# Optimization experiments

Measured on AMD Instinct MI355X. Metric: run time of the kernel, lower is better.

The kernel has to match this reference:

```python
import jax, jax.numpy as jnp
import numpy as np


def _hungarian(cost):
    """Kuhn-Munkres / Jonker-Volgenant shortest augmenting path on a square
    cost matrix (numpy, float). Returns col index assigned to each row,
    identical to scipy.optimize.linear_sum_assignment's col_ind."""
    n = cost.shape[0]
    INF = np.inf
    u = np.zeros(n + 1)
    v = np.zeros(n + 1)
    p = np.zeros(n + 1, dtype=np.int64)    # p[j] = row matched to col j (1-based)
    way = np.zeros(n + 1, dtype=np.int64)
    for i in range(1, n + 1):
        p[0] = i
        j0 = 0
        minv = np.full(n + 1, INF)
        used = np.zeros(n + 1, dtype=bool)
        while True:
            used[j0] = True
            i0 = p[j0]
            cur = cost[i0 - 1] - u[i0] - v[1:]
            m1 = minv[1:]
            w1 = way[1:]
            upd = (~used[1:]) & (cur < m1)
            m1[upd] = cur[upd]
            w1[upd] = j0
            masked = np.where(used[1:], INF, m1)
            j1 = int(np.argmin(masked)) + 1
            delta = masked[j1 - 1]
            uidx = np.nonzero(used)[0]
            u[p[uidx]] += delta
            v[uidx] -= delta
            minv[~used] -= delta
            j0 = j1
            if p[j0] == 0:
                break
        # augment along the alternating path
        while True:
            j1 = way[j0]
            p[j0] = p[j1]
            j0 = j1
            if j0 == 0:
                break
    ans = np.zeros(n, dtype=np.int64)
    for j in range(1, n + 1):
        ans[p[j] - 1] = j - 1
    return ans


def _cdist(a, b):
    # [B,K,D] x [B,K,D] -> [B,K,K] pairwise L2 distances (torch.cdist p=2)
    aa = jnp.sum(a * a, axis=-1)[:, :, None]
    bb = jnp.sum(b * b, axis=-1)[:, None, :]
    ab = jnp.einsum('bkd,bjd->bkj', a, b)
    return jnp.sqrt(jnp.clip(aa + bb - 2.0 * ab, 0.0))


def setup_inputs() -> dict:
    key = jax.random.key(0)
    k1, k2, k3 = jax.random.split(key, 3)
    B, K, D, N = 64, 32, 256, 16384
    return {
        'slots_t': jax.random.normal(k1, (B, K, D), jnp.float32),
        'slots_t1': jax.random.normal(k2, (B, K, D), jnp.float32),
        'masks_t': jax.random.uniform(k3, (B, N, K), jnp.float32),
    }


def reference(slots_t, slots_t1, masks_t):
    # cost matrix (l2) and per-batch optimal assignment (host-side, like torch)
    cost = np.asarray(_cdist(slots_t, slots_t1))          # [B,K,K]
    match = jnp.asarray(
        np.stack([_hungarian(cost[b]) for b in range(cost.shape[0])]))  # [B,K]
    # gather matched slots from t+1
    matched = jnp.take_along_axis(slots_t1, match[:, :, None], axis=1)  # [B,K,D]
    loss = jnp.sum((slots_t - matched) ** 2, axis=-1)                   # [B,K]
    # slot-utilization weighting from masks
    util = masks_t.sum(axis=1)                                          # [B,K]
    util = util / util.sum(axis=1, keepdims=True)
    loss = loss * util
    return loss.mean()
```

## Files before the change

kernel.cpp:

```cpp
#include <hip/hip_runtime.h>
#include <math.h>

#define BATCH 64
#define KSL   32
#define DIM   256
#define NMASK 16384

template<int CTRL>
__device__ __forceinline__ double dpp_mov_f64(double x) {
  union { double d; int i[2]; } a, r;
  a.d = x;
  r.i[0] = __builtin_amdgcn_update_dpp(a.i[0], a.i[0], CTRL, 0xF, 0xF, false);
  r.i[1] = __builtin_amdgcn_update_dpp(a.i[1], a.i[1], CTRL, 0xF, 0xF, false);
  return r.d;
}

__device__ __forceinline__ double readlane_f64(double x, int lane) {
  union { double d; unsigned long long u; } a; a.d = x;
  int lo = __builtin_amdgcn_readlane((int)(a.u & 0xFFFFFFFFull), lane);
  int hi = __builtin_amdgcn_readlane((int)(a.u >> 32), lane);
  union { unsigned long long u; double d; } r;
  r.u = ((unsigned long long)(unsigned)hi << 32) | (unsigned)lo;
  return r.d;
}

__global__ __launch_bounds__(256) void fused_kernel(
    const float* __restrict__ slots_t, const float* __restrict__ slots_t1,
    const float* __restrict__ masks,
    int* __restrict__ match, float* __restrict__ partial) {
  int tid = threadIdx.x;
  if (blockIdx.x < BATCH) {
    int b = blockIdx.x;
    __shared__ float as[KSL][64];
    __shared__ float bs[KSL][65];
    __shared__ float cs[KSL][KSL];
    const float* ab = slots_t  + (size_t)b * KSL * DIM;
    const float* bb = slots_t1 + (size_t)b * KSL * DIM;

    float acc[4] = {0.f, 0.f, 0.f, 0.f};
    for (int c = 0; c < DIM / 64; ++c) {
      __syncthreads();
      for (int e = tid; e < KSL * 64; e += 256) {
        int kk = e >> 6, dd = e & 63;
        as[kk][dd] = ab[kk * DIM + c * 64 + dd];
        bs[kk][dd] = bb[kk * DIM + c * 64 + dd];
      }
      __syncthreads();
      #pragma unroll
      for (int p4 = 0; p4 < 4; ++p4) {
        int id = p4 * 256 + tid;
        int i = id >> 5, j = id & 31;
        float s = acc[p4];
        #pragma unroll
        for (int dd = 0; dd < 64; ++dd) {
          float df = as[i][dd] - bs[j][dd];
          s = fmaf(df, df, s);
        }
        acc[p4] = s;
      }
    }
    __syncthreads();
    #pragma unroll
    for (int p4 = 0; p4 < 4; ++p4) {
      int id = p4 * 256 + tid;
      cs[id >> 5][id & 31] = sqrtf(acc[p4]);
    }
    __syncthreads();
    if (tid >= 32) return;

    const int col = tid;
    double v = 0.0, up = 0.0;
    int pcol = 0;
    unsigned freemask = 0xFFFFFFFFu;
    for (int i = 1; i <= KSL; ++i) {
      double u_i = 0.0;
      int used = 0;
      int i0 = i;
      double u0 = 0.0;
      for (;;) {
        double cur = (double)cs[i0 - 1][col] - u0 - v;
        double masked = used ? __builtin_inf() : cur;
        double m = masked;
        m = fmin(m, dpp_mov_f64<0xB1>(m));
        m = fmin(m, dpp_mov_f64<0x4E>(m));
        m = fmin(m, dpp_mov_f64<0x141>(m));
        m = fmin(m, dpp_mov_f64<0x140>(m));
        m = fmin(m, dpp_mov_f64<0x142>(m));
        double delta = readlane_f64(m, 31);
        unsigned eq = (unsigned)__ballot(masked == delta);
        int j1c = __builtin_amdgcn_readfirstlane(__ffs(eq) - 1);
        double u0n = readlane_f64(up, j1c);
        int    i0n = __builtin_amdgcn_readlane(pcol, j1c);
        if (used) { up += delta; v -= delta; }
        u_i += delta;
        if (freemask & (1u << j1c)) {
          if (col == j1c) { pcol = i; up = u_i; }
          freemask &= ~(1u << j1c);
          break;
        }
        if (col == j1c) used = 1;
        u0 = u0n;
        i0 = i0n;
      }
    }
    match[b * KSL + (pcol - 1)] = col;
  } else {
    int idx = blockIdx.x - BATCH;
    int b = idx >> 5, chunk = idx & 31;
    const int ROWS = NMASK / 32;
    const float4* m4 = (const float4*)(masks + (size_t)b * NMASK * KSL +
                                       (size_t)chunk * ROWS * KSL);
    int q = tid & 7;
    int r = tid >> 3;
    float4 acc4 = make_float4(0.f, 0.f, 0.f, 0.f);
    for (int rr = r; rr < ROWS; rr += 32) {
      float4 t = m4[rr * 8 + q];
      acc4.x += t.x; acc4.y += t.y; acc4.z += t.z; acc4.w += t.w;
    }
    __shared__ float red[256][4];
    red[tid][0] = acc4.x; red[tid][1] = acc4.y;
    red[tid][2] = acc4.z; red[tid][3] = acc4.w;
    __syncthreads();
    if (tid < KSL) {
      int qq = tid >> 2, c = tid & 3;
      float s = 0.f;
      for (int g = 0; g < 32; ++g) s += red[g * 8 + qq][c];
      partial[(size_t)b * 1024 + chunk * 32 + tid] = s;
    }
  }
}

__global__ __launch_bounds__(256) void final_kernel(
    const float* __restrict__ st, const float* __restrict__ st1,
    const int* __restrict__ match, const float* __restrict__ partial,
    float* __restrict__ bloss) {
  int b = blockIdx.x, tid = threadIdx.x;
  __shared__ float util[KSL], ls[KSL], red[256];
  if (tid < KSL) {
    float s = 0.f;
    for (int c = 0; c < 32; ++c) s += partial[(size_t)b * 1024 + c * 32 + tid];
    util[tid] = s;
  }
  int k = tid >> 3, l8 = tid & 7;
  int mk = match[b * KSL + k];
  const float* x = st  + ((size_t)b * KSL + k)  * DIM;
  const float* y = st1 + ((size_t)b * KSL + mk) * DIM;
  float acc = 0.f;
  for (int d = l8; d < DIM; d += 8) {
    float df = x[d] - y[d];
    acc = fmaf(df, df, acc);
  }
  red[tid] = acc;
  __syncthreads();
  if (l8 == 0) {
    float s = 0.f;
    #pragma unroll
    for (int t = 0; t < 8; ++t) s += red[tid + t];
    ls[k] = s;
  }
  __syncthreads();
  if (tid == 0) {
    float us = 0.f;
    for (int kk = 0; kk < KSL; ++kk) us += util[kk];
    float s = 0.f;
    for (int kk = 0; kk < KSL; ++kk) s += ls[kk] * (util[kk] / us);
    bloss[b] = s;
  }
}

__global__ void reduce_kernel(const float* __restrict__ bloss,
                              float* __restrict__ out) {
  float v = bloss[threadIdx.x];
  #pragma unroll
  for (int off = 32; off > 0; off >>= 1) v += __shfl_down(v, off);
  if (threadIdx.x == 0) out[0] = v / (float)(BATCH * KSL);
}

extern "C" void kernel_launch(void* const* d_in, const int* in_sizes, int n_in,
                              void* d_out, int out_size, void* d_ws, size_t ws_size,
                              hipStream_t stream) {
  const float* slots_t  = (const float*)d_in[0];
  const float* slots_t1 = (const float*)d_in[1];
  const float* masks    = (const float*)d_in[2];

  char* ws = (char*)d_ws;
  int*   match   = (int*)  (ws);
  float* partial = (float*)(ws + 2048 * 4);
  float* bloss   = (float*)(ws + 2048 * 4 + 65536 * 4);

  fused_kernel<<<BATCH + BATCH * 32, 256, 0, stream>>>(slots_t, slots_t1, masks,
                                                       match, partial);
  final_kernel<<<BATCH, 256, 0, stream>>>(slots_t, slots_t1, match, partial, bloss);
  reduce_kernel<<<1, 64, 0, stream>>>(bloss, (float*)d_out);
}
```

Before: 63.86 us.

## Fuse assignment, mask reduction and loss into one per-batch kernel

Merges the cost/Hungarian kernel, the mask-utilization reduction and the final loss kernel into a single 512-thread block per batch. One wavefront runs the Hungarian solve while the other seven wavefronts reduce the full mask slab for that batch, so the two overlap. The solve now keeps each cost column in registers and picks rows with a select tree instead of reading shared memory. The loss gather uses float4 loads and a shuffle reduction. This removes the partial-sum and match buffers in global memory and one kernel launch. The cost is that the 134 MB mask read is now spread over only 64 blocks instead of about two thousand, which risks leaving memory bandwidth badly underused.

```diff
diff --git a/kernel.cpp b/kernel.cpp
--- a/kernel.cpp
+++ b/kernel.cpp
@@ -24,139 +24,148 @@
   return r.d;
 }
 
-__global__ __launch_bounds__(256) void fused_kernel(
+__device__ __forceinline__ float sel32(const float (&cc)[KSL], int idx) {
+  float l0[16], l1[8], l2[4], l3[2];
+  bool b4 = (idx & 16) != 0;
+  #pragma unroll
+  for (int r = 0; r < 16; ++r) l0[r] = b4 ? cc[r + 16] : cc[r];
+  bool b3 = (idx & 8) != 0;
+  #pragma unroll
+  for (int r = 0; r < 8; ++r) l1[r] = b3 ? l0[r + 8] : l0[r];
+  bool b2 = (idx & 4) != 0;
+  #pragma unroll
+  for (int r = 0; r < 4; ++r) l2[r] = b2 ? l1[r + 4] : l1[r];
+  bool b1 = (idx & 2) != 0;
+  #pragma unroll
+  for (int r = 0; r < 2; ++r) l3[r] = b1 ? l2[r + 2] : l2[r];
+  return (idx & 1) ? l3[1] : l3[0];
+}
+
+__global__ __launch_bounds__(512) void batch_kernel(
     const float* __restrict__ slots_t, const float* __restrict__ slots_t1,
-    const float* __restrict__ masks,
-    int* __restrict__ match, float* __restrict__ partial) {
-  int tid = threadIdx.x;
-  if (blockIdx.x < BATCH) {
-    int b = blockIdx.x;
-    __shared__ float as[KSL][64];
-    __shared__ float bs[KSL][65];
-    __shared__ float cs[KSL][KSL];
-    const float* ab = slots_t  + (size_t)b * KSL * DIM;
-    const float* bb = slots_t1 + (size_t)b * KSL * DIM;
+    const float* __restrict__ masks, float* __restrict__ bloss) {
+  int b = blockIdx.x, tid = threadIdx.x;
+  __shared__ float as[KSL][64];
+  __shared__ float bs[KSL][65];
+  __shared__ float cs[KSL][KSL];
+  __shared__ float red[448][4];
+  __shared__ float util[KSL], ls[KSL];
+  __shared__ int   sh_match[KSL];
 
-    float acc[4] = {0.f, 0.f, 0.f, 0.f};
-    for (int c = 0; c < DIM / 64; ++c) {
-      __syncthreads();
-      for (int e = tid; e < KSL * 64; e += 256) {
-        int kk = e >> 6, dd = e & 63;
-        as[kk][dd] = ab[kk * DIM + c * 64 + dd];
-        bs[kk][dd] = bb[kk * DIM + c * 64 + dd];
-      }
-      __syncthreads();
-      #pragma unroll
-      for (int p4 = 0; p4 < 4; ++p4) {
-        int id = p4 * 256 + tid;
-        int i = id >> 5, j = id & 31;
-        float s = acc[p4];
-        #pragma unroll
-        for (int dd = 0; dd < 64; ++dd) {
-          float df = as[i][dd] - bs[j][dd];
-          s = fmaf(df, df, s);
-        }
-        acc[p4] = s;
-      }
+  const float* ab = slots_t  + (size_t)b * KSL * DIM;
+  const float* bb = slots_t1 + (size_t)b * KSL * DIM;
+
+  float acc[2] = {0.f, 0.f};
+  for (int c = 0; c < DIM / 64; ++c) {
+    __syncthreads();
+    for (int e = tid; e < KSL * 64; e += 512) {
+      int kk = e >> 6, dd = e & 63;
+      as[kk][dd] = ab[kk * DIM + c * 64 + dd];
+      bs[kk][dd] = bb[kk * DIM + c * 64 + dd];
     }
     __syncthreads();
     #pragma unroll
-    for (int p4 = 0; p4 < 4; ++p4) {
-      int id = p4 * 256 + tid;
-      cs[id >> 5][id & 31] = sqrtf(acc[p4]);
-    }
-    __syncthreads();
-    if (tid >= 32) return;
-
-    const int col = tid;
-    double v = 0.0, up = 0.0;
-    int pcol = 0;
-    unsigned freemask = 0xFFFFFFFFu;
-    for (int i = 1; i <= KSL; ++i) {
-      double u_i = 0.0;
-      int used = 0;
-      int i0 = i;
-      double u0 = 0.0;
-      for (;;) {
-        double cur = (double)cs[i0 - 1][col] - u0 - v;
-        double masked = used ? __builtin_inf() : cur;
-        double m = masked;
-        m = fmin(m, dpp_mov_f64<0xB1>(m));
-        m = fmin(m, dpp_mov_f64<0x4E>(m));
-        m = fmin(m, dpp_mov_f64<0x141>(m));
-        m = fmin(m, dpp_mov_f64<0x140>(m));
-        m = fmin(m, dpp_mov_f64<0x142>(m));
-        double delta = readlane_f64(m, 31);
-        unsigned eq = (unsigned)__ballot(masked == delta);
-        int j1c = __builtin_amdgcn_readfirstlane(__ffs(eq) - 1);
-        double u0n = readlane_f64(up, j1c);
-        int    i0n = __builtin_amdgcn_readlane(pcol, j1c);
-        if (used) { up += delta; v -= delta; }
-        u_i += delta;
-        if (freemask & (1u << j1c)) {
-          if (col == j1c) { pcol = i; up = u_i; }
-          freemask &= ~(1u << j1c);
-          break;
-        }
-        if (col == j1c) used = 1;
-        u0 = u0n;
-        i0 = i0n;
+    for (int p4 = 0; p4 < 2; ++p4) {
+      int id = p4 * 512 + tid;
+      int i = id >> 5, j = id & 31;
+      float s = acc[p4];
+      #pragma unroll
+      for (int dd = 0; dd < 64; ++dd) {
+        float df = as[i][dd] - bs[j][dd];
+        s = fmaf(df, df, s);
       }
-    }
-    match[b * KSL + (pcol - 1)] = col;
-  } else {
-    int idx = blockIdx.x - BATCH;
-    int b = idx >> 5, chunk = idx & 31;
-    const int ROWS = NMASK / 32;
-    const float4* m4 = (const float4*)(masks + (size_t)b * NMASK * KSL +
-                                       (size_t)chunk * ROWS * KSL);
-    int q = tid & 7;
-    int r = tid >> 3;
-    float4 acc4 = make_float4(0.f, 0.f, 0.f, 0.f);
-    for (int rr = r; rr < ROWS; rr += 32) {
-      float4 t = m4[rr * 8 + q];
-      acc4.x += t.x; acc4.y += t.y; acc4.z += t.z; acc4.w += t.w;
-    }
-    __shared__ float red[256][4];
-    red[tid][0] = acc4.x; red[tid][1] = acc4.y;
-    red[tid][2] = acc4.z; red[tid][3] = acc4.w;
-    __syncthreads();
-    if (tid < KSL) {
-      int qq = tid >> 2, c = tid & 3;
-      float s = 0.f;
-      for (int g = 0; g < 32; ++g) s += red[g * 8 + qq][c];
-      partial[(size_t)b * 1024 + chunk * 32 + tid] = s;
+      acc[p4] = s;
     }
   }
-}
+  __syncthreads();
+  #pragma unroll
+  for (int p4 = 0; p4 < 2; ++p4) {
+    int id = p4 * 512 + tid;
+    cs[id >> 5][id & 31] = sqrtf(acc[p4]);
+  }
+  __syncthreads();
 
-__global__ __launch_bounds__(256) void final_kernel(
-    const float* __restrict__ st, const float* __restrict__ st1,
-    const int* __restrict__ match, const float* __restrict__ partial,
-    float* __restrict__ bloss) {
-  int b = blockIdx.x, tid = threadIdx.x;
-  __shared__ float util[KSL], ls[KSL], red[256];
+  if (tid < 64) {
+    if (tid < KSL) {
+      const int col = tid;
+      float cc[KSL];
+      #pragma unroll
+      for (int r = 0; r < KSL; ++r) cc[r] = cs[r][col];
+      const double INF = __builtin_inf();
+      double v = 0.0, up = 0.0;
+      int pcol = 0;
+      for (int i = 1; i <= KSL; ++i) {
+        double u_i = 0.0;
+        int used = 0;
+        double cur0 = (double)sel32(cc, i - 1);
+        for (;;) {
+          double cur = cur0 - v;
+          double masked = used ? INF : cur;
+          double m = masked;
+          m = fmin(m, dpp_mov_f64<0xB1>(m));
+          m = fmin(m, dpp_mov_f64<0x4E>(m));
+          m = fmin(m, dpp_mov_f64<0x141>(m));
+          m = fmin(m, dpp_mov_f64<0x140>(m));
+          m = fmin(m, dpp_mov_f64<0x142>(m));
+          double delta = readlane_f64(m, 31);
+          unsigned eq = (unsigned)__ballot(masked == delta);
+          int j1c = __builtin_amdgcn_readfirstlane(__ffs(eq) - 1);
+          int i0n = __builtin_amdgcn_readlane(pcol, j1c);
+          double u0n = readlane_f64(up, j1c);
+          int rown = (i0n > 0) ? (i0n - 1) : 0;
+          double cur0n = (double)sel32(cc, rown) - u0n;
+          if (used) { up += delta; v -= delta; }
+          u_i += delta;
+          if (i0n == 0) {
+            if (col == j1c) { pcol = i; up = u_i; }
+            break;
+          }
+          if (col == j1c) used = 1;
+          cur0 = cur0n;
+        }
+      }
+      sh_match[pcol - 1] = col;
+    }
+  } else {
+    int idx = tid - 64;
+    int q = idx & 7;
+    int r = idx >> 3;
+    const float4* m4 = (const float4*)(masks + (size_t)b * NMASK * KSL);
+    float4 a4 = make_float4(0.f, 0.f, 0.f, 0.f);
+    #pragma unroll 4
+    for (int rr = r; rr < NMASK; rr += 56) {
+      float4 t = m4[rr * 8 + q];
+      a4.x += t.x; a4.y += t.y; a4.z += t.z; a4.w += t.w;
+    }
+    red[idx][0] = a4.x; red[idx][1] = a4.y;
+    red[idx][2] = a4.z; red[idx][3] = a4.w;
+  }
+  __syncthreads();
+
   if (tid < KSL) {
+    int q = tid >> 2, c = tid & 3;
     float s = 0.f;
-    for (int c = 0; c < 32; ++c) s += partial[(size_t)b * 1024 + c * 32 + tid];
+    for (int g = 0; g < 56; ++g) s += red[g * 8 + q][c];
     util[tid] = s;
   }
-  int k = tid >> 3, l8 = tid & 7;
-  int mk = match[b * KSL + k];
-  const float* x = st  + ((size_t)b * KSL + k)  * DIM;
-  const float* y = st1 + ((size_t)b * KSL + mk) * DIM;
-  float acc = 0.f;
-  for (int d = l8; d < DIM; d += 8) {
-    float df = x[d] - y[d];
-    acc = fmaf(df, df, acc);
-  }
-  red[tid] = acc;
-  __syncthreads();
-  if (l8 == 0) {
+  {
+    int k = tid >> 4, l16 = tid & 15;
+    int mk = sh_match[k];
+    const float4* x4 = (const float4*)(ab + k * DIM);
+    const float4* y4 = (const float4*)(bb + mk * DIM);
     float s = 0.f;
     #pragma unroll
-    for (int t = 0; t < 8; ++t) s += red[tid + t];
-    ls[k] = s;
+    for (int d = 0; d < 4; ++d) {
+      float4 xv = x4[l16 + d * 16];
+      float4 yv = y4[l16 + d * 16];
+      float dx = xv.x - yv.x, dy = xv.y - yv.y;
+      float dz = xv.z - yv.z, dw = xv.w - yv.w;
+      s = fmaf(dx, dx, s); s = fmaf(dy, dy, s);
+      s = fmaf(dz, dz, s); s = fmaf(dw, dw, s);
+    }
+    #pragma unroll
+    for (int off = 8; off > 0; off >>= 1) s += __shfl_down(s, off, 16);
+    if (l16 == 0) ls[k] = s;
   }
   __syncthreads();
   if (tid == 0) {
@@ -183,13 +192,8 @@
   const float* slots_t1 = (const float*)d_in[1];
   const float* masks    = (const float*)d_in[2];
 
-  char* ws = (char*)d_ws;
-  int*   match   = (int*)  (ws);
-  float* partial = (float*)(ws + 2048 * 4);
-  float* bloss   = (float*)(ws + 2048 * 4 + 65536 * 4);
+  float* bloss = (float*)d_ws;
 
-  fused_kernel<<<BATCH + BATCH * 32, 256, 0, stream>>>(slots_t, slots_t1, masks,
-                                                       match, partial);
-  final_kernel<<<BATCH, 256, 0, stream>>>(slots_t, slots_t1, match, partial, bloss);
+  batch_kernel<<<BATCH, 512, 0, stream>>>(slots_t, slots_t1, masks, bloss);
   reduce_kernel<<<1, 64, 0, stream>>>(bloss, (float*)d_out);
 }
```

New measurement: 149.9 us. 135% more time.

## Register-cache cost column in Hungarian loop and fold final reduce into last block

Applied to the files above, without the earlier changes.

Each lane of the Hungarian wave now keeps its cost column in registers and selects rows with a branchless mux tree. The next row's cost is prefetched in the same iteration, which takes LDS loads off the serial augmenting-path loop. The free-column test now uses the matched-row value read from the lane instead of a separate bitmask. The separate reduce kernel is replaced by an atomic counter so the last final block does the global sum. This saves one launch but adds a memset, and the fused kernel gets launch_bounds(256,2), which may raise register pressure.

```diff
diff --git a/kernel.cpp b/kernel.cpp
--- a/kernel.cpp
+++ b/kernel.cpp
@@ -24,7 +24,24 @@
   return r.d;
 }
 
-__global__ __launch_bounds__(256) void fused_kernel(
+__device__ __forceinline__ float sel32(const float (&cc)[KSL], int idx) {
+  float l0[16], l1[8], l2[4], l3[2];
+  bool b4 = (idx & 16) != 0;
+  #pragma unroll
+  for (int r = 0; r < 16; ++r) l0[r] = b4 ? cc[r + 16] : cc[r];
+  bool b3 = (idx & 8) != 0;
+  #pragma unroll
+  for (int r = 0; r < 8; ++r) l1[r] = b3 ? l0[r + 8] : l0[r];
+  bool b2 = (idx & 4) != 0;
+  #pragma unroll
+  for (int r = 0; r < 4; ++r) l2[r] = b2 ? l1[r + 4] : l1[r];
+  bool b1 = (idx & 2) != 0;
+  #pragma unroll
+  for (int r = 0; r < 2; ++r) l3[r] = b1 ? l2[r + 2] : l2[r];
+  return (idx & 1) ? l3[1] : l3[0];
+}
+
+__global__ __launch_bounds__(256, 2) void fused_kernel(
     const float* __restrict__ slots_t, const float* __restrict__ slots_t1,
     const float* __restrict__ masks,
     int* __restrict__ match, float* __restrict__ partial) {
@@ -33,7 +50,7 @@
     int b = blockIdx.x;
     __shared__ float as[KSL][64];
     __shared__ float bs[KSL][65];
-    __shared__ float cs[KSL][KSL];
+    __shared__ float cs[KSL][33];
     const float* ab = slots_t  + (size_t)b * KSL * DIM;
     const float* bb = slots_t1 + (size_t)b * KSL * DIM;
 
@@ -69,17 +86,19 @@
     if (tid >= 32) return;
 
     const int col = tid;
+    float cc[KSL];
+    #pragma unroll
+    for (int r = 0; r < KSL; ++r) cc[r] = cs[r][col];
+    const double INF = __builtin_inf();
     double v = 0.0, up = 0.0;
     int pcol = 0;
-    unsigned freemask = 0xFFFFFFFFu;
     for (int i = 1; i <= KSL; ++i) {
       double u_i = 0.0;
       int used = 0;
-      int i0 = i;
-      double u0 = 0.0;
+      double cur0 = (double)sel32(cc, i - 1);
       for (;;) {
-        double cur = (double)cs[i0 - 1][col] - u0 - v;
-        double masked = used ? __builtin_inf() : cur;
+        double cur = cur0 - v;
+        double masked = used ? INF : cur;
         double m = masked;
         m = fmin(m, dpp_mov_f64<0xB1>(m));
         m = fmin(m, dpp_mov_f64<0x4E>(m));
@@ -89,18 +108,18 @@
         double delta = readlane_f64(m, 31);
         unsigned eq = (unsigned)__ballot(masked == delta);
         int j1c = __builtin_amdgcn_readfirstlane(__ffs(eq) - 1);
+        int i0n = __builtin_amdgcn_readlane(pcol, j1c);
         double u0n = readlane_f64(up, j1c);
-        int    i0n = __builtin_amdgcn_readlane(pcol, j1c);
+        int rown = (i0n > 0) ? (i0n - 1) : 0;
+        double cur0n = (double)sel32(cc, rown) - u0n;
         if (used) { up += delta; v -= delta; }
         u_i += delta;
-        if (freemask & (1u << j1c)) {
+        if (i0n == 0) {
           if (col == j1c) { pcol = i; up = u_i; }
-          freemask &= ~(1u << j1c);
           break;
         }
         if (col == j1c) used = 1;
-        u0 = u0n;
-        i0 = i0n;
+        cur0 = cur0n;
       }
     }
     match[b * KSL + (pcol - 1)] = col;
@@ -112,14 +131,14 @@
                                        (size_t)chunk * ROWS * KSL);
     int q = tid & 7;
     int r = tid >> 3;
-    float4 acc4 = make_float4(0.f, 0.f, 0.f, 0.f);
+    float4 a4 = make_float4(0.f, 0.f, 0.f, 0.f);
     for (int rr = r; rr < ROWS; rr += 32) {
       float4 t = m4[rr * 8 + q];
-      acc4.x += t.x; acc4.y += t.y; acc4.z += t.z; acc4.w += t.w;
+      a4.x += t.x; a4.y += t.y; a4.z += t.z; a4.w += t.w;
     }
     __shared__ float red[256][4];
-    red[tid][0] = acc4.x; red[tid][1] = acc4.y;
-    red[tid][2] = acc4.z; red[tid][3] = acc4.w;
+    red[tid][0] = a4.x; red[tid][1] = a4.y;
+    red[tid][2] = a4.z; red[tid][3] = a4.w;
     __syncthreads();
     if (tid < KSL) {
       int qq = tid >> 2, c = tid & 3;
@@ -130,12 +149,14 @@
   }
 }
 
-__global__ __launch_bounds__(256) void final_kernel(
+__global__ __launch_bounds__(256) void finale_kernel(
     const float* __restrict__ st, const float* __restrict__ st1,
     const int* __restrict__ match, const float* __restrict__ partial,
-    float* __restrict__ bloss) {
+    float* __restrict__ bloss, unsigned* __restrict__ counter,
+    float* __restrict__ out) {
   int b = blockIdx.x, tid = threadIdx.x;
   __shared__ float util[KSL], ls[KSL], red[256];
+  __shared__ int sh_last;
   if (tid < KSL) {
     float s = 0.f;
     for (int c = 0; c < 32; ++c) s += partial[(size_t)b * 1024 + c * 32 + tid];
@@ -165,15 +186,18 @@
     float s = 0.f;
     for (int kk = 0; kk < KSL; ++kk) s += ls[kk] * (util[kk] / us);
     bloss[b] = s;
-  }
-}
-
-__global__ void reduce_kernel(const float* __restrict__ bloss,
-                              float* __restrict__ out) {
-  float v = bloss[threadIdx.x];
-  #pragma unroll
-  for (int off = 32; off > 0; off >>= 1) v += __shfl_down(v, off);
-  if (threadIdx.x == 0) out[0] = v / (float)(BATCH * KSL);
+    __threadfence();
+    unsigned old = atomicAdd(counter, 1u);
+    sh_last = (old == BATCH - 1) ? 1 : 0;
+  }
+  __syncthreads();
+  if (sh_last && tid < 64) {
+    __threadfence();
+    float v = atomicAdd(&bloss[tid], 0.0f);
+    #pragma unroll
+    for (int off = 32; off > 0; off >>= 1) v += __shfl_down(v, off);
+    if (tid == 0) out[0] = v / (float)(BATCH * KSL);
+  }
 }
 
 extern "C" void kernel_launch(void* const* d_in, const int* in_sizes, int n_in,
@@ -184,12 +208,14 @@
   const float* masks    = (const float*)d_in[2];
 
   char* ws = (char*)d_ws;
-  int*   match   = (int*)  (ws);
-  float* partial = (float*)(ws + 2048 * 4);
-  float* bloss   = (float*)(ws + 2048 * 4 + 65536 * 4);
-
+  int*      match   = (int*)     (ws);
+  float*    partial = (float*)   (ws + 8192);
+  float*    bloss   = (float*)   (ws + 8192 + 262144);
+  unsigned* counter = (unsigned*)(ws + 8192 + 262144 + 256);
+
+  hipMemsetAsync(counter, 0, sizeof(unsigned), stream);
   fused_kernel<<<BATCH + BATCH * 32, 256, 0, stream>>>(slots_t, slots_t1, masks,
                                                        match, partial);
-  final_kernel<<<BATCH, 256, 0, stream>>>(slots_t, slots_t1, match, partial, bloss);
-  reduce_kernel<<<1, 64, 0, stream>>>(bloss, (float*)d_out);
-}
+  finale_kernel<<<BATCH, 256, 0, stream>>>(slots_t, slots_t1, match, partial,
+                                           bloss, counter, (float*)d_out);
+}
```

Result: slower. 173.2 us (+171.2%).
